# Performance work log

Hardware: AMD Instinct MI355X
Metric: run time of the kernel (lower is better)

The kernel has to match this reference:

```python
import jax, jax.numpy as jnp
import numpy as np
from jax import lax

B, CIN, COUT, H, W = 16, 256, 128, 32, 32
KD = 3   # deformable conv kernel
KU = 4
PAD = 1  # deform conv padding
EPS = 1e-5


def setup_inputs() -> dict:
    key = jax.random.key(0)
    ks = jax.random.split(key, 5)
    s3 = 1.0 / np.sqrt(CIN * KD * KD)
    s_up = 1.0 / np.sqrt(COUT * KU * KU)
    return {
        "x": jax.random.normal(ks[0], (B, CIN, H, W), jnp.float32),
        "w_off": jax.random.normal(ks[1], (3 * KD * KD, CIN, KD, KD), jnp.float32) * s3,
        "b_off": jnp.zeros((3 * KD * KD,), jnp.float32),
        "w_dcn": jax.random.normal(ks[2], (COUT, CIN, KD, KD), jnp.float32) * s3,
        "b_dcn": jnp.zeros((COUT,), jnp.float32),
        "g1": jnp.ones((COUT,), jnp.float32),
        "bt1": jnp.zeros((COUT,), jnp.float32),
        "w_up": jax.random.normal(ks[3], (COUT, COUT, KU, KU), jnp.float32) * s_up,  # torch ConvTranspose2d weight layout (in, out, kh, kw)
        "g2": jnp.ones((COUT,), jnp.float32),
        "bt2": jnp.zeros((COUT,), jnp.float32),
    }


def _conv3x3(x, w, b):
    y = lax.conv_general_dilated(x, w, (1, 1), [(1, 1), (1, 1)],
                                 dimension_numbers=("NCHW", "OIHW", "NCHW"))
    return y + b[None, :, None, None]


def _bn_relu(x, g, b):
    # training-mode BatchNorm2d: batch stats over (N, H, W), biased variance
    mu = jnp.mean(x, (0, 2, 3), keepdims=True)
    var = jnp.var(x, (0, 2, 3), keepdims=True)
    y = (x - mu) * lax.rsqrt(var + EPS)
    return jax.nn.relu(y * g[None, :, None, None] + b[None, :, None, None])


def _deform_conv(x, offset, mask, w, b):
    # modulated deformable conv v2, matching torchvision.ops.DeformConv2d
    Bb, C, Hh, Ww = x.shape
    Kk = KD * KD
    off = offset.reshape(Bb, Kk, 2, Hh, Ww)
    dy, dx = off[:, :, 0], off[:, :, 1]          # [B, Kk, H, W]
    ky, kx = jnp.meshgrid(jnp.arange(KD), jnp.arange(KD), indexing="ij")
    ky = (ky.reshape(-1) - PAD).astype(x.dtype)  # [Kk]
    kx = (kx.reshape(-1) - PAD).astype(x.dtype)
    ii = jnp.arange(Hh, dtype=x.dtype)[None, None, :, None]
    jj = jnp.arange(Ww, dtype=x.dtype)[None, None, None, :]
    py = ii + ky[None, :, None, None] + dy       # [B, Kk, H, W] sample rows
    px = jj + kx[None, :, None, None] + dx       # [B, Kk, H, W] sample cols
    y0 = jnp.floor(py)
    x0 = jnp.floor(px)
    wy = py - y0
    wx = px - x0
    HW = Hh * Ww
    x_flat = x.reshape(Bb, 1, C, HW)

    def corner(yc, xc, wgt):
        valid = (yc >= 0) & (yc <= Hh - 1) & (xc >= 0) & (xc <= Ww - 1)
        yi = jnp.clip(yc, 0, Hh - 1).astype(jnp.int32)
        xi = jnp.clip(xc, 0, Ww - 1).astype(jnp.int32)
        idx = (yi * Ww + xi).reshape(Bb, Kk, 1, HW)
        v = jnp.take_along_axis(x_flat, jnp.broadcast_to(idx, (Bb, Kk, C, HW)), axis=-1)
        wv = (wgt * valid.astype(x.dtype)).reshape(Bb, Kk, 1, HW)
        return v * wv

    samp = (corner(y0, x0, (1 - wy) * (1 - wx)) + corner(y0, x0 + 1, (1 - wy) * wx)
            + corner(y0 + 1, x0, wy * (1 - wx)) + corner(y0 + 1, x0 + 1, wy * wx))
    samp = samp * mask.reshape(Bb, Kk, 1, HW)    # [B, Kk, C, HW]
    out = jnp.einsum("bkcp,ock->bop", samp, w.reshape(w.shape[0], C, Kk))
    return out.reshape(Bb, -1, Hh, Ww) + b[None, :, None, None]


def reference(x, w_off, b_off, w_dcn, b_dcn, g1, bt1, w_up, g2, bt2):
    off = _conv3x3(x, w_off, b_off)              # [B, 27, H, W]
    Kk = KD * KD
    o1, o2, m = off[:, :Kk], off[:, Kk:2 * Kk], off[:, 2 * Kk:]
    offset = jnp.concatenate([o1, o2], axis=1)   # [B, 18, H, W], torchvision pair layout
    mask = jax.nn.sigmoid(m)
    y = _deform_conv(x, offset, mask, w_dcn, b_dcn)
    y = _bn_relu(y, g1, bt1)
    # ConvTranspose2d(k=4, s=2, p=1): conv over lhs-dilated input with flipped kernel
    w_t = jnp.flip(w_up, (2, 3)).transpose(1, 0, 2, 3)  # (out, in, kh, kw)
    p = KU - 1 - 1  # k - 1 - deconv_pad
    y = lax.conv_general_dilated(y, w_t, (1, 1), [(p, p), (p, p)],
                                 lhs_dilation=(2, 2),
                                 dimension_numbers=("NCHW", "OIHW", "NCHW"))
    return _bn_relu(y, g2, bt2)
```

## Files before the change

### kernel.cpp

```cpp
#include <hip/hip_runtime.h>
#include <hip/hip_fp16.h>
#include <math.h>

#define HW 1024
#define EPSV 1e-5f

typedef unsigned int uint;
typedef unsigned short ushort;
typedef __attribute__((ext_vector_type(8))) short short8;
typedef __attribute__((ext_vector_type(8))) _Float16 half8;
typedef __attribute__((ext_vector_type(4))) float floatx4;

static const size_t BOFF = 0;
static const size_t BD   = 36864;
static const size_t BQ   = 184320;
static const size_t XT   = 315392;
static const size_t OFFB = 2412544;
static const size_t ST1  = 2936832;
static const size_t ST2  = 2937856;
static const size_t YP   = 2941952;
static const size_t YSUM = 7136256;
static const size_t YBN  = 8184832;
static const size_t OB   = 9233408;

__device__ inline ushort f2bf(float f) {
  uint u = __builtin_bit_cast(uint, f);
  uint r = (u + 0x7FFFu + ((u >> 16) & 1u)) >> 16;
  return (ushort)r;
}
__device__ inline float b2f(ushort u) {
  return __builtin_bit_cast(float, ((uint)u) << 16);
}

__global__ __launch_bounds__(256) void prep_xt_kernel(const float* __restrict__ x,
                                                      const float* __restrict__ w_off,
                                                      const float* __restrict__ w_dcn,
                                                      const float* __restrict__ w_up,
                                                      float* __restrict__ ws) {
  __shared__ float tile[64 * 65];
  int blk = blockIdx.x;
  int tid = threadIdx.x;
  if (blk < 1024) {
    int b = blk & 15, pt = (blk >> 4) & 15, cc = blk >> 8;
    int p0 = pt * 64, c0 = cc * 64;
    int pp4 = tid & 15, ci = tid >> 4;
#pragma unroll
    for (int it = 0; it < 4; ++it) {
      int c = it * 16 + ci;
      float4 v = *(const float4*)(x + ((size_t)(b * 256 + c0 + c)) * HW + p0 + pp4 * 4);
      tile[c * 65 + pp4 * 4 + 0] = v.x;
      tile[c * 65 + pp4 * 4 + 1] = v.y;
      tile[c * 65 + pp4 * 4 + 2] = v.z;
      tile[c * 65 + pp4 * 4 + 3] = v.w;
    }
    __syncthreads();
    int cp = tid & 31, pp2 = tid >> 5;
    uint* xtu = (uint*)(ws + XT);
#pragma unroll
    for (int it = 0; it < 8; ++it) {
      int p = it * 8 + pp2;
      __half2 h = __floats2half2_rn(tile[(2 * cp) * 65 + p], tile[(2 * cp + 1) * 65 + p]);
      xtu[(size_t)(b * 1024 + p0 + p) * 128 + cc * 32 + cp] = __builtin_bit_cast(uint, h);
    }
  } else if (blk < 3488) {
    int i = (blk - 1024) * 256 + tid;
    if (i < 73728) {
      int c = i & 255; int n = (i >> 8) & 31; int tap = i >> 13;
      float v = (n < 27) ? w_off[((size_t)n * 256 + c) * 9 + tap] : 0.f;
      ((__half*)(ws + BOFF))[i] = __float2half(v);
    } else if (i < 73728 + 294912) {
      int d = i - 73728;
      int oc = d / 2304; int k = d % 2304;
      int tap = k >> 8; int c = k & 255;
      ((__half*)(ws + BD))[d] = __float2half(w_dcn[((size_t)oc * 256 + c) * 9 + tap]);
    } else if (i < 73728 + 294912 + 262144) {
      int d = i - (73728 + 294912);
      int j = d & 7; int n = (d >> 3) & 127; int quad = (d >> 10) & 3;
      int kstep = (d >> 12) & 15; int par = d >> 16;
      int k = kstep * 32 + quad * 8 + j;
      int t4 = k >> 7; int c = k & 127;
      int ty = t4 >> 1, tx = t4 & 1;
      int pu = par >> 1, pv = par & 1;
      int ky = (1 - pu) + 2 * ty, kx = (1 - pv) + 2 * tx;
      float v = w_up[((size_t)c * 128 + n) * 16 + ky * 4 + kx];
      ((ushort*)(ws + BQ))[d] = f2bf(v);
    }
  } else {
    int i = (blk - 3488) * 256 + tid;
    if (i < 5120) ws[ST1 + i] = 0.f;
    else if (i < 5120 + 524288) ws[OFFB + (i - 5120)] = 0.f;
  }
}

__global__ __launch_bounds__(256) void offconv_mfma_kernel(const __half* __restrict__ xt,
                                                           const __half* __restrict__ boff,
                                                           float* __restrict__ off) {
  __shared__ short As[32 * 132];
  __shared__ short Bs[32 * 132];
  int blk = blockIdx.x;
  int b = blk & 15, cs = (blk >> 4) & 1, pt = blk >> 5;
  int P0 = pt * 32;
  int tid = threadIdx.x;
  int wid = tid >> 6, lane = tid & 63, lr = lane & 15, quad = lane >> 4;
  int m_w = (wid & 1) * 16, n_w = (wid >> 1) * 16;
  int arow = tid >> 3, aseg = tid & 7;
  int pix = P0 + arow; int h = pix >> 5, w = pix & 31;

  floatx4 acc = (floatx4)0.f;

  for (int tap = 0; tap < 9; ++tap) {
    int ty = tap / 3, tx = tap % 3;
    int yy = h + ty - 1, xx = w + tx - 1;
    bool valid = (yy >= 0) && (yy < 32) && (xx >= 0) && (xx < 32);
    int pos = min(max(yy, 0), 31) * 32 + min(max(xx, 0), 31);
    const float4* ga = (const float4*)(xt + ((size_t)(b * 1024 + pos)) * 256 + cs * 128 + aseg * 16);
    float4 a0 = ga[0], a1 = ga[1];
    if (!valid) { a0 = make_float4(0.f, 0.f, 0.f, 0.f); a1 = a0; }
    const float4* gb = (const float4*)(boff + ((size_t)(tap * 32 + arow)) * 256 + cs * 128 + aseg * 16);
    float4 b0 = gb[0], b1 = gb[1];
    if (tap) __syncthreads();
    float4* qa = (float4*)(As + arow * 132 + aseg * 16);
    qa[0] = a0; qa[1] = a1;
    float4* qb = (float4*)(Bs + arow * 132 + aseg * 16);
    qb[0] = b0; qb[1] = b1;
    __syncthreads();
#pragma unroll
    for (int k2 = 0; k2 < 4; ++k2) {
      half8 af = *(const half8*)(As + (m_w + lr) * 132 + k2 * 32 + quad * 8);
      half8 bf = *(const half8*)(Bs + (n_w + lr) * 132 + k2 * 32 + quad * 8);
      acc = __builtin_amdgcn_mfma_f32_16x16x32_f16(af, bf, acc, 0, 0, 0);
    }
  }
  int n = n_w + lr;
#pragma unroll
  for (int r = 0; r < 4; ++r) {
    int m = m_w + quad * 4 + r;
    atomicAdd(&off[((size_t)(b * 1024 + P0 + m)) * 32 + n], acc[r]);
  }
}

__global__ __launch_bounds__(256) void deform_mfma_kernel(const __half* __restrict__ xt,
                                                          const float* __restrict__ off,
                                                          const float* __restrict__ b_off,
                                                          const __half* __restrict__ bd,
                                                          ushort* __restrict__ y_part) {
  __shared__ short As[64 * 72];
  __shared__ short Bs[128 * 72];
  int blk = blockIdx.x;
  int b = blk & 15;
  int rr = blk >> 4;
  int ptile = rr & 15, cs = rr >> 4;
  int tid = threadIdx.x;
  int wid = tid >> 6, lane = tid & 63, lr = lane & 15, quad = lane >> 4;
  int m_w = (wid & 1) * 32, n_w = (wid >> 1) * 64;
  int P0 = ptile * 64;
  int pix_l = tid >> 2, cseg = tid & 3;
  int pix = P0 + pix_l;
  int h = pix >> 5, w = pix & 31;
  const float* offb = off + (size_t)(b * 1024 + pix) * 32;
  const __half* xb = xt + (size_t)b * 1024 * 256 + cs * 64 + cseg * 16;
  int ocb = tid >> 1, seg = tid & 1;
  const __half* bdr = bd + (size_t)ocb * 2304 + cs * 64 + seg * 32;

  float4 o4[7];
#pragma unroll
  for (int i = 0; i < 7; ++i) o4[i] = ((const float4*)offb)[i];
  float oflat[28];
#pragma unroll
  for (int i = 0; i < 7; ++i) {
    oflat[4 * i] = o4[i].x; oflat[4 * i + 1] = o4[i].y;
    oflat[4 * i + 2] = o4[i].z; oflat[4 * i + 3] = o4[i].w;
  }

  floatx4 acc[2][4];
#pragma unroll
  for (int mi = 0; mi < 2; ++mi)
#pragma unroll
    for (int ni = 0; ni < 4; ++ni) acc[mi][ni] = (floatx4)0.f;

#pragma unroll
  for (int tap = 0; tap < 9; ++tap) {
    float dy = oflat[2 * tap] + b_off[2 * tap];
    float dx = oflat[2 * tap + 1] + b_off[2 * tap + 1];
    float mraw = oflat[18 + tap] + b_off[18 + tap];
    float mm = 1.f / (1.f + __expf(-mraw));
    float py = (float)(h + tap / 3 - 1) + dy;
    float px = (float)(w + tap % 3 - 1) + dx;
    float y0f = floorf(py), x0f = floorf(px);
    float wy = py - y0f, wx = px - x0f;
    int y0 = (int)y0f, x0 = (int)x0f;
    float cw[4] = {(1.f - wy) * (1.f - wx), (1.f - wy) * wx, wy * (1.f - wx), wy * wx};
    uint4 q[4][2];
    __half2 w2[4];
#pragma unroll
    for (int t = 0; t < 4; ++t) {
      int yy = y0 + (t >> 1), xx = x0 + (t & 1);
      bool v = (yy >= 0) && (yy <= 31) && (xx >= 0) && (xx <= 31);
      int yc = min(max(yy, 0), 31), xc = min(max(xx, 0), 31);
      const uint4* xr = (const uint4*)(xb + (size_t)(yc * 32 + xc) * 256);
      q[t][0] = xr[0]; q[t][1] = xr[1];
      w2[t] = __float2half2_rn(v ? cw[t] * mm : 0.f);
    }
    const float4* gb = (const float4*)(bdr + tap * 256);
    float4 b0 = gb[0], b1 = gb[1], b2 = gb[2], b3 = gb[3];

    __half2 hacc[8];
#pragma unroll
    for (int j = 0; j < 8; ++j) hacc[j] = __float2half2_rn(0.f);
#pragma unroll
    for (int t = 0; t < 4; ++t) {
      uint qa[8] = {q[t][0].x, q[t][0].y, q[t][0].z, q[t][0].w,
                    q[t][1].x, q[t][1].y, q[t][1].z, q[t][1].w};
#pragma unroll
      for (int j = 0; j < 8; ++j)
        hacc[j] = __hfma2(w2[t], __builtin_bit_cast(__half2, qa[j]), hacc[j]);
    }
    if (tap) __syncthreads();
    {
      float4 f0, f1;
      f0.x = __builtin_bit_cast(float, hacc[0]);
      f0.y = __builtin_bit_cast(float, hacc[1]);
      f0.z = __builtin_bit_cast(float, hacc[2]);
      f0.w = __builtin_bit_cast(float, hacc[3]);
      f1.x = __builtin_bit_cast(float, hacc[4]);
      f1.y = __builtin_bit_cast(float, hacc[5]);
      f1.z = __builtin_bit_cast(float, hacc[6]);
      f1.w = __builtin_bit_cast(float, hacc[7]);
      float4* qa2 = (float4*)(As + pix_l * 72 + cseg * 16);
      qa2[0] = f0; qa2[1] = f1;
    }
    float4* qb = (float4*)(Bs + ocb * 72 + seg * 32);
    qb[0] = b0; qb[1] = b1; qb[2] = b2; qb[3] = b3;
    __syncthreads();
#pragma unroll
    for (int k2 = 0; k2 < 2; ++k2) {
      half8 af[2], bf[4];
#pragma unroll
      for (int mi = 0; mi < 2; ++mi)
        af[mi] = *(const half8*)(As + (m_w + mi * 16 + lr) * 72 + k2 * 32 + quad * 8);
#pragma unroll
      for (int ni = 0; ni < 4; ++ni)
        bf[ni] = *(const half8*)(Bs + (n_w + ni * 16 + lr) * 72 + k2 * 32 + quad * 8);
#pragma unroll
      for (int mi = 0; mi < 2; ++mi)
#pragma unroll
        for (int ni = 0; ni < 4; ++ni)
          acc[mi][ni] = __builtin_amdgcn_mfma_f32_16x16x32_f16(af[mi], bf[ni], acc[mi][ni], 0, 0, 0);
    }
  }
  ushort* yp = y_part + (size_t)cs * 2097152 + ((size_t)(b * 1024 + P0)) * 128;
#pragma unroll
  for (int mi = 0; mi < 2; ++mi) {
#pragma unroll
    for (int r = 0; r < 4; ++r) {
      int m = m_w + mi * 16 + quad * 4 + r;
      ushort* orow = yp + (size_t)m * 128;
#pragma unroll
      for (int ni = 0; ni < 4; ++ni)
        orow[n_w + ni * 16 + lr] = f2bf(acc[mi][ni][r]);
    }
  }
}

__global__ __launch_bounds__(256) void yred_kernel(const ushort* __restrict__ yp,
                                                   const float* __restrict__ b_dcn,
                                                   ushort* __restrict__ ysum,
                                                   float* __restrict__ st1) {
  int blk = blockIdx.x;
  int b = blk & 15, seg = blk >> 4;
  int tid = threadIdx.x;
  int px = tid >> 4, ocg = tid & 15;
  int lane = tid & 63, wid = tid >> 6;
  size_t idx = ((size_t)(b * 1024 + seg * 16 + px)) * 128 + ocg * 8;
  short8 p0 = *(const short8*)(yp + idx);
  short8 p1 = *(const short8*)(yp + 2097152 + idx);
  short8 p2 = *(const short8*)(yp + 4194304 + idx);
  short8 p3 = *(const short8*)(yp + 6291456 + idx);
  float s[8], q[8];
  short8 ov;
#pragma unroll
  for (int j = 0; j < 8; ++j) {
    float v = b2f((ushort)p0[j]) + b2f((ushort)p1[j]) + b2f((ushort)p2[j])
            + b2f((ushort)p3[j]) + b_dcn[ocg * 8 + j];
    ov[j] = (short)f2bf(v);
    s[j] = v; q[j] = v * v;
  }
  *(short8*)(ysum + idx) = ov;
#pragma unroll
  for (int j = 0; j < 8; ++j) {
    s[j] += __shfl_xor(s[j], 16); s[j] += __shfl_xor(s[j], 32);
    q[j] += __shfl_xor(q[j], 16); q[j] += __shfl_xor(q[j], 32);
  }
  __shared__ float red[4][256];
  if (lane < 16) {
#pragma unroll
    for (int j = 0; j < 8; ++j) {
      red[wid][lane * 8 + j] = s[j];
      red[wid][128 + lane * 8 + j] = q[j];
    }
  }
  __syncthreads();
  float tot = red[0][tid] + red[1][tid] + red[2][tid] + red[3][tid];
  atomicAdd(&st1[(blk & 3) * 256 + tid], tot);
}

__global__ __launch_bounds__(256) void ybn_kernel(const ushort* __restrict__ ysum,
                                                  const float* __restrict__ st1,
                                                  const float* __restrict__ g1,
                                                  const float* __restrict__ bt1,
                                                  ushort* __restrict__ ybn) {
  __shared__ float scs[128], shs[128];
  int tid = threadIdx.x;
  if (tid < 128) {
    float s  = st1[tid] + st1[256 + tid] + st1[512 + tid] + st1[768 + tid];
    float sq = st1[128 + tid] + st1[384 + tid] + st1[640 + tid] + st1[896 + tid];
    float mean = s / 16384.f;
    float var = sq / 16384.f - mean * mean;
    float sc = g1[tid] * rsqrtf(var + EPSV);
    scs[tid] = sc;
    shs[tid] = fmaf(-mean, sc, bt1[tid]);
  }
  __syncthreads();
  int blk = blockIdx.x;
  int b = blk & 15, seg = blk >> 4;
  int i8 = (b * 64 + seg) * 256 + tid;
  size_t i = (size_t)i8 * 8;
  int oc = (int)(i & 127);
  uint4 pv = *(const uint4*)(ysum + i);
  uint words[4] = {pv.x, pv.y, pv.z, pv.w};
  uint owords[4];
#pragma unroll
  for (int j = 0; j < 4; ++j) {
    ushort u0 = (ushort)(words[j] & 0xFFFFu);
    ushort u1 = (ushort)(words[j] >> 16);
    int c0 = oc + 2 * j, c1 = oc + 2 * j + 1;
    float v0 = fmaxf(fmaf(b2f(u0), scs[c0], shs[c0]), 0.f);
    float v1 = fmaxf(fmaf(b2f(u1), scs[c1], shs[c1]), 0.f);
    owords[j] = (uint)f2bf(v0) | ((uint)f2bf(v1) << 16);
  }
  *(uint4*)(ybn + i) = make_uint4(owords[0], owords[1], owords[2], owords[3]);
}

__global__ __launch_bounds__(256) void deconv_mfma_kernel(const ushort* __restrict__ ybn,
                                                          const ushort* __restrict__ bq,
                                                          ushort* __restrict__ O,
                                                          float* __restrict__ st2) {
  int blk = blockIdx.x;
  int b = blk & 15, par = (blk >> 4) & 3, pt = blk >> 6;
  int pu = par >> 1, pv = par & 1;
  int tid = threadIdx.x;
  int wid = tid >> 6, lane = tid & 63, lr = lane & 15, quad = lane >> 4;
  int P0 = pt * 64;
  int hh[4], ww[4];
#pragma unroll
  for (int mi = 0; mi < 4; ++mi) {
    int p = P0 + mi * 16 + lr;
    hh[mi] = p >> 5; ww[mi] = p & 31;
  }

  floatx4 acc[4][2];
#pragma unroll
  for (int mi = 0; mi < 4; ++mi)
#pragma unroll
    for (int ni = 0; ni < 2; ++ni) acc[mi][ni] = (floatx4)0.f;

  const ushort* ybb = ybn + (size_t)b * 1024 * 128;
  const ushort* bqb = bq + par * 65536 + quad * 1024 + (wid * 32 + lr) * 8;

#pragma unroll
  for (int tap = 0; tap < 4; ++tap) {
    int ty = tap >> 1, tx = tap & 1;
    int ab[4]; bool val[4];
#pragma unroll
    for (int mi = 0; mi < 4; ++mi) {
      int i = hh[mi] + pu - ty, j = ww[mi] + pv - tx;
      val[mi] = (i >= 0) && (i <= 31) && (j >= 0) && (j <= 31);
      int pos = min(max(i, 0), 31) * 32 + min(max(j, 0), 31);
      ab[mi] = pos * 128;
    }
#pragma unroll
    for (int k2 = 0; k2 < 4; ++k2) {
      int kstep = tap * 4 + k2;
      int c0 = k2 * 32 + quad * 8;
      short8 bf[2];
#pragma unroll
      for (int ni = 0; ni < 2; ++ni)
        bf[ni] = *(const short8*)(bqb + kstep * 4096 + ni * 128);
      short8 af[4];
#pragma unroll
      for (int mi = 0; mi < 4; ++mi) {
        short8 a = *(const short8*)(ybb + ab[mi] + c0);
        af[mi] = val[mi] ? a : (short8)0;
      }
#pragma unroll
      for (int mi = 0; mi < 4; ++mi)
#pragma unroll
        for (int ni = 0; ni < 2; ++ni)
          acc[mi][ni] = __builtin_amdgcn_mfma_f32_16x16x32_bf16(af[mi], bf[ni], acc[mi][ni], 0, 0, 0);
    }
  }
  size_t obase = (size_t)(b * 4 + par) * 1024 * 128;
#pragma unroll
  for (int mi = 0; mi < 4; ++mi) {
#pragma unroll
    for (int r = 0; r < 4; ++r) {
      int m = mi * 16 + quad * 4 + r;
      ushort* orow = O + obase + (size_t)(P0 + m) * 128 + wid * 32;
#pragma unroll
      for (int ni = 0; ni < 2; ++ni)
        orow[ni * 16 + lr] = f2bf(acc[mi][ni][r]);
    }
  }
  float sn[2], qn[2];
#pragma unroll
  for (int ni = 0; ni < 2; ++ni) {
    float s = 0.f, q = 0.f;
#pragma unroll
    for (int mi = 0; mi < 4; ++mi)
#pragma unroll
      for (int r = 0; r < 4; ++r) {
        float v = acc[mi][ni][r];
        s += v; q = fmaf(v, v, q);
      }
    sn[ni] = s; qn[ni] = q;
  }
#pragma unroll
  for (int ni = 0; ni < 2; ++ni) {
    sn[ni] += __shfl_xor(sn[ni], 16);
    sn[ni] += __shfl_xor(sn[ni], 32);
    qn[ni] += __shfl_xor(qn[ni], 16);
    qn[ni] += __shfl_xor(qn[ni], 32);
  }
  if (lane < 16) {
    float* dst = st2 + pt * 256;
#pragma unroll
    for (int ni = 0; ni < 2; ++ni) {
      atomicAdd(&dst[wid * 32 + ni * 16 + lr], sn[ni]);
      atomicAdd(&dst[128 + wid * 32 + ni * 16 + lr], qn[ni]);
    }
  }
}

__global__ __launch_bounds__(256) void bnout_kernel(const ushort* __restrict__ O,
                                                    const float* __restrict__ st2,
                                                    const float* __restrict__ g2,
                                                    const float* __restrict__ bt2,
                                                    float* __restrict__ out) {
  __shared__ float tile[128 * 33];
  __shared__ float scs[128], shs[128];
  int blk = blockIdx.x;
  int b = blk & 15, par = (blk >> 4) & 3, uu = blk >> 6;
  int pu = par >> 1, pv = par & 1;
  int tid = threadIdx.x;
  if (tid < 128) {
    float s = 0.f, sq = 0.f;
#pragma unroll
    for (int c = 0; c < 16; ++c) {
      s += st2[c * 256 + tid];
      sq += st2[c * 256 + 128 + tid];
    }
    float mean = s / 65536.f;
    float var = sq / 65536.f - mean * mean;
    float sc = g2[tid] * rsqrtf(var + EPSV);
    scs[tid] = sc;
    shs[tid] = fmaf(-mean, sc, bt2[tid]);
  }
  __syncthreads();
#pragma unroll 4
  for (int it = 0; it < 16; ++it) {
    int idx = it * 256 + tid;
    int vv = idx >> 7, oc = idx & 127;
    float v = b2f(O[((size_t)(b * 4 + par) * 1024 + uu * 32 + vv) * 128 + oc]);
    tile[oc * 33 + vv] = fmaxf(fmaf(v, scs[oc], shs[oc]), 0.f);
  }
  __syncthreads();
#pragma unroll 4
  for (int it = 0; it < 16; ++it) {
    int idx = it * 256 + tid;
    int oc = idx >> 5, vv = idx & 31;
    out[((size_t)b * 128 + oc) * 4096 + (2 * uu + pu) * 64 + 2 * vv + pv] = tile[oc * 33 + vv];
  }
}

extern "C" void kernel_launch(void* const* d_in, const int* in_sizes, int n_in,
                              void* d_out, int out_size, void* d_ws, size_t ws_size,
                              hipStream_t stream) {
  const float* x     = (const float*)d_in[0];
  const float* w_off = (const float*)d_in[1];
  const float* b_off = (const float*)d_in[2];
  const float* w_dcn = (const float*)d_in[3];
  const float* b_dcn = (const float*)d_in[4];
  const float* g1    = (const float*)d_in[5];
  const float* bt1   = (const float*)d_in[6];
  const float* w_up  = (const float*)d_in[7];
  const float* g2    = (const float*)d_in[8];
  const float* bt2   = (const float*)d_in[9];
  float* ws  = (float*)d_ws;
  float* out = (float*)d_out;

  prep_xt_kernel<<<5556, 256, 0, stream>>>(x, w_off, w_dcn, w_up, ws);
  offconv_mfma_kernel<<<1024, 256, 0, stream>>>((const __half*)(ws + XT),
                                                (const __half*)(ws + BOFF), ws + OFFB);
  deform_mfma_kernel<<<1024, 256, 0, stream>>>((const __half*)(ws + XT), ws + OFFB, b_off,
                                               (const __half*)(ws + BD), (ushort*)(ws + YP));
  yred_kernel<<<1024, 256, 0, stream>>>((const ushort*)(ws + YP), b_dcn,
                                        (ushort*)(ws + YSUM), ws + ST1);
  ybn_kernel<<<1024, 256, 0, stream>>>((const ushort*)(ws + YSUM), ws + ST1, g1, bt1,
                                       (ushort*)(ws + YBN));
  deconv_mfma_kernel<<<1024, 256, 0, stream>>>((const ushort*)(ws + YBN),
                                               (const ushort*)(ws + BQ),
                                               (ushort*)(ws + OB), ws + ST2);
  bnout_kernel<<<2048, 256, 0, stream>>>((const ushort*)(ws + OB), ws + ST2, g2, bt2, out);
}
```

Measured before the change: 195.0 us.

## Read offconv weights directly from global and vectorize BN-out stores across both column parities

The offset-conv kernel stops staging weight tiles in shared memory and has each lane load its MFMA B fragment straight from global memory, which drops one LDS write and read per tap. The final BN+ReLU kernel now handles both column parities in one block, so it can read four bf16 values per load and write full contiguous 64-float output rows with float4 stores instead of stride-2 scalar stores. This halves the grid and doubles the tile per block. The direct global weight reads depend on L1/L2 caching because they are re-read by many blocks.

```diff
diff --git a/kernel.cpp b/kernel.cpp
--- a/kernel.cpp
+++ b/kernel.cpp
@@ -96,7 +96,6 @@
                                                            const __half* __restrict__ boff,
                                                            float* __restrict__ off) {
   __shared__ short As[32 * 132];
-  __shared__ short Bs[32 * 132];
   int blk = blockIdx.x;
   int b = blk & 15, cs = (blk >> 4) & 1, pt = blk >> 5;
   int P0 = pt * 32;
@@ -105,6 +104,7 @@
   int m_w = (wid & 1) * 16, n_w = (wid >> 1) * 16;
   int arow = tid >> 3, aseg = tid & 7;
   int pix = P0 + arow; int h = pix >> 5, w = pix & 31;
+  const __half* bb = boff + (size_t)(n_w + lr) * 256 + cs * 128 + quad * 8;
 
   floatx4 acc = (floatx4)0.f;
 
@@ -116,18 +116,15 @@
     const float4* ga = (const float4*)(xt + ((size_t)(b * 1024 + pos)) * 256 + cs * 128 + aseg * 16);
     float4 a0 = ga[0], a1 = ga[1];
     if (!valid) { a0 = make_float4(0.f, 0.f, 0.f, 0.f); a1 = a0; }
-    const float4* gb = (const float4*)(boff + ((size_t)(tap * 32 + arow)) * 256 + cs * 128 + aseg * 16);
-    float4 b0 = gb[0], b1 = gb[1];
     if (tap) __syncthreads();
     float4* qa = (float4*)(As + arow * 132 + aseg * 16);
     qa[0] = a0; qa[1] = a1;
-    float4* qb = (float4*)(Bs + arow * 132 + aseg * 16);
-    qb[0] = b0; qb[1] = b1;
     __syncthreads();
+    const __half* brow = bb + (size_t)(tap * 32) * 256;
 #pragma unroll
     for (int k2 = 0; k2 < 4; ++k2) {
       half8 af = *(const half8*)(As + (m_w + lr) * 132 + k2 * 32 + quad * 8);
-      half8 bf = *(const half8*)(Bs + (n_w + lr) * 132 + k2 * 32 + quad * 8);
+      half8 bf = *(const half8*)(brow + k2 * 32);
       acc = __builtin_amdgcn_mfma_f32_16x16x32_f16(af, bf, acc, 0, 0, 0);
     }
   }
@@ -446,11 +443,10 @@
                                                     const float* __restrict__ g2,
                                                     const float* __restrict__ bt2,
                                                     float* __restrict__ out) {
-  __shared__ float tile[128 * 33];
+  __shared__ float tile[128 * 68];
   __shared__ float scs[128], shs[128];
   int blk = blockIdx.x;
-  int b = blk & 15, par = (blk >> 4) & 3, uu = blk >> 6;
-  int pu = par >> 1, pv = par & 1;
+  int b = blk & 15, pu = (blk >> 4) & 1, uu = blk >> 5;
   int tid = threadIdx.x;
   if (tid < 128) {
     float s = 0.f, sq = 0.f;
@@ -466,19 +462,31 @@
     shs[tid] = fmaf(-mean, sc, bt2[tid]);
   }
   __syncthreads();
-#pragma unroll 4
-  for (int it = 0; it < 16; ++it) {
-    int idx = it * 256 + tid;
-    int vv = idx >> 7, oc = idx & 127;
-    float v = b2f(O[((size_t)(b * 4 + par) * 1024 + uu * 32 + vv) * 128 + oc]);
-    tile[oc * 33 + vv] = fmaxf(fmaf(v, scs[oc], shs[oc]), 0.f);
+#pragma unroll
+  for (int it = 0; it < 8; ++it) {
+    int linear = it * 256 + tid;
+    int ocg = linear & 31;
+    int vv = (linear >> 5) & 31;
+    int pv = linear >> 10;
+    const ushort* src = O + ((size_t)(b * 4 + 2 * pu + pv) * 1024 + uu * 32 + vv) * 128 + ocg * 4;
+    uint2 u = *(const uint2*)src;
+    int col = 2 * vv + pv;
+    int oc0 = ocg * 4;
+    ushort e0 = (ushort)(u.x & 0xFFFFu), e1 = (ushort)(u.x >> 16);
+    ushort e2 = (ushort)(u.y & 0xFFFFu), e3 = (ushort)(u.y >> 16);
+    tile[(oc0 + 0) * 68 + col] = fmaxf(fmaf(b2f(e0), scs[oc0 + 0], shs[oc0 + 0]), 0.f);
+    tile[(oc0 + 1) * 68 + col] = fmaxf(fmaf(b2f(e1), scs[oc0 + 1], shs[oc0 + 1]), 0.f);
+    tile[(oc0 + 2) * 68 + col] = fmaxf(fmaf(b2f(e2), scs[oc0 + 2], shs[oc0 + 2]), 0.f);
+    tile[(oc0 + 3) * 68 + col] = fmaxf(fmaf(b2f(e3), scs[oc0 + 3], shs[oc0 + 3]), 0.f);
   }
   __syncthreads();
-#pragma unroll 4
-  for (int it = 0; it < 16; ++it) {
-    int idx = it * 256 + tid;
-    int oc = idx >> 5, vv = idx & 31;
-    out[((size_t)b * 128 + oc) * 4096 + (2 * uu + pu) * 64 + 2 * vv + pv] = tile[oc * 33 + vv];
+  int row = 2 * uu + pu;
+#pragma unroll
+  for (int it = 0; it < 8; ++it) {
+    int oc = it * 16 + (tid >> 4);
+    int c4 = (tid & 15) * 4;
+    float4 v = *(const float4*)&tile[oc * 68 + c4];
+    *(float4*)(out + ((size_t)(b * 128 + oc)) * 4096 + row * 64 + c4) = v;
   }
 }
 
@@ -510,5 +518,5 @@
   deconv_mfma_kernel<<<1024, 256, 0, stream>>>((const ushort*)(ws + YBN),
                                                (const ushort*)(ws + BQ),
                                                (ushort*)(ws + OB), ws + ST2);
-  bnout_kernel<<<2048, 256, 0, stream>>>((const ushort*)(ws + OB), ws + ST2, g2, bt2, out);
-}
+  bnout_kernel<<<1024, 256, 0, stream>>>((const ushort*)(ws + OB), ws + ST2, g2, bt2, out);
+}
```

After: 199.8 us. 1.02x slower.
